# Performance work log

Measured on AMD Instinct MI355X. Metric: run time of the kernel, lower is better.

Reference implementation:

```python
import jax, jax.numpy as jnp
import numpy as np

EMBED_DIM = 1024
NUM_HEADS = 16
HEAD_DIM = EMBED_DIM // NUM_HEADS
MLP_HIDDEN = 4096
B, S = 2, 2048


def setup_inputs() -> dict:
    key = jax.random.key(0)
    ks = jax.random.split(key, 10)
    sd = lambda fan_in: 1.0 / np.sqrt(fan_in)
    x = jax.random.normal(ks[0], (B, S, EMBED_DIM), dtype=jnp.float32)
    # weights stored (in, out) so y = x @ W + b (same math as torch Linear)
    w_qkv = jax.random.normal(ks[1], (EMBED_DIM, 3 * EMBED_DIM), jnp.float32) * sd(EMBED_DIM)
    w_proj = jax.random.normal(ks[2], (EMBED_DIM, EMBED_DIM), jnp.float32) * sd(EMBED_DIM)
    b_proj = jnp.zeros((EMBED_DIM,), jnp.float32)
    w_fc1 = jax.random.normal(ks[3], (EMBED_DIM, MLP_HIDDEN), jnp.float32) * sd(EMBED_DIM)
    b_fc1 = jnp.zeros((MLP_HIDDEN,), jnp.float32)
    w_fc2 = jax.random.normal(ks[4], (MLP_HIDDEN, EMBED_DIM), jnp.float32) * sd(MLP_HIDDEN)
    b_fc2 = jnp.zeros((EMBED_DIM,), jnp.float32)
    g1 = jnp.ones((EMBED_DIM,), jnp.float32)
    be1 = jnp.zeros((EMBED_DIM,), jnp.float32)
    g2 = jnp.ones((EMBED_DIM,), jnp.float32)
    be2 = jnp.zeros((EMBED_DIM,), jnp.float32)
    return {"x": x, "w_qkv": w_qkv, "w_proj": w_proj, "b_proj": b_proj,
            "w_fc1": w_fc1, "b_fc1": b_fc1, "w_fc2": w_fc2, "b_fc2": b_fc2,
            "g1": g1, "be1": be1, "g2": g2, "be2": be2}


def _layernorm(x, g, b, eps=1e-5):
    mu = jnp.mean(x, axis=-1, keepdims=True)
    var = jnp.var(x, axis=-1, keepdims=True)
    return (x - mu) * jax.lax.rsqrt(var + eps) * g + b


def _block(x, w_qkv, w_proj, b_proj, w_fc1, b_fc1, w_fc2, b_fc2, g1, be1, g2, be2):
    # --- attention branch ---
    h = _layernorm(x, g1, be1)
    qkv = h @ w_qkv  # [B,S,3D]
    qkv = qkv.reshape(B, S, 3, NUM_HEADS, HEAD_DIM).transpose(2, 0, 3, 1, 4)
    q, k, v = qkv[0], qkv[1], qkv[2]  # each [B,H,S,Dh]
    scale = 1.0 / np.sqrt(HEAD_DIM).astype(np.float32)
    dots = jnp.einsum('bhqd,bhkd->bhqk', q, k) * scale  # naive full score matrix
    attn = jax.nn.softmax(dots, axis=-1)
    out = jnp.einsum('bhqk,bhkd->bhqd', attn, v)
    out = out.transpose(0, 2, 1, 3).reshape(B, S, EMBED_DIM)
    x = x + (out @ w_proj + b_proj)
    # --- mlp branch ---
    h2 = _layernorm(x, g2, be2)
    mlp = jax.nn.gelu(h2 @ w_fc1 + b_fc1, approximate=False) @ w_fc2 + b_fc2
    return x + mlp


def reference(x, w_qkv, w_proj, b_proj, w_fc1, b_fc1, w_fc2, b_fc2, g1, be1, g2, be2):
    return _block(x, w_qkv, w_proj, b_proj, w_fc1, b_fc1, w_fc2, b_fc2, g1, be1, g2, be2)
```

## Files before the change

kernel.cpp:

```cpp
#include <hip/hip_runtime.h>

typedef __attribute__((ext_vector_type(8))) short short8;
typedef __attribute__((ext_vector_type(4))) float f32x4;

#define MFMA16(a, b, c) __builtin_amdgcn_mfma_f32_16x16x32_bf16((a), (b), (c), 0, 0, 0)

static __device__ __forceinline__ unsigned short f2bf(float f) {
    unsigned int u = __float_as_uint(f);
    return (unsigned short)((u + 0x7fffu + ((u >> 16) & 1u)) >> 16);
}

static __device__ __forceinline__ void glds16(const unsigned short* g, unsigned short* l) {
    __builtin_amdgcn_global_load_lds(
        (const __attribute__((address_space(1))) unsigned int*)g,
        (__attribute__((address_space(3))) unsigned int*)l, 16, 0, 0);
}

__global__ __launch_bounds__(256) void convt_all_kernel(
    const float* __restrict__ w_qkv, const float* __restrict__ w_proj,
    const float* __restrict__ w_fc1, const float* __restrict__ w_fc2,
    unsigned short* __restrict__ wqkvT, unsigned short* __restrict__ wprojT,
    unsigned short* __restrict__ wfc1T, unsigned short* __restrict__ wfc2T) {
    __shared__ unsigned short Ts[32][33];
    int id = blockIdx.x;
    const float* W; unsigned short* WT; int K, N, bx, by;
    if (id < 3072)      { W = w_qkv;  WT = wqkvT;  K = 1024; N = 3072; bx = id % 96;  by = id / 96; }
    else if (id < 4096) { id -= 3072; W = w_proj; WT = wprojT; K = 1024; N = 1024; bx = id & 31; by = id >> 5; }
    else if (id < 8192) { id -= 4096; W = w_fc1;  WT = wfc1T;  K = 1024; N = 4096; bx = id & 127; by = id >> 7; }
    else                { id -= 8192; W = w_fc2;  WT = wfc2T;  K = 4096; N = 1024; bx = id & 31; by = id >> 5; }
    int t = threadIdx.x;
    int bk = by * 32, bn = bx * 32;
    int r = t >> 3, c = (t & 7) * 4;
    float4 w = *(const float4*)&W[(size_t)(bk + r) * N + bn + c];
    Ts[c + 0][r] = f2bf(w.x); Ts[c + 1][r] = f2bf(w.y);
    Ts[c + 2][r] = f2bf(w.z); Ts[c + 3][r] = f2bf(w.w);
    __syncthreads();
    ushort4 o;
    o.x = Ts[r][c]; o.y = Ts[r][c + 1]; o.z = Ts[r][c + 2]; o.w = Ts[r][c + 3];
    *(ushort4*)&WT[(size_t)(bn + r) * K + bk + c] = o;
}

__global__ __launch_bounds__(256) void ln_kernel(const float* __restrict__ x,
                                                 const float* __restrict__ g,
                                                 const float* __restrict__ be,
                                                 unsigned short* __restrict__ y) {
    int row = blockIdx.x;
    const float* xr = x + (size_t)row * 1024;
    unsigned short* yr = y + (size_t)row * 1024;
    int t = threadIdx.x;
    float v[4];
    float sum = 0.f, sq = 0.f;
#pragma unroll
    for (int i = 0; i < 4; ++i) {
        float f = xr[t + i * 256];
        v[i] = f; sum += f; sq += f * f;
    }
#pragma unroll
    for (int o = 32; o > 0; o >>= 1) { sum += __shfl_down(sum, o); sq += __shfl_down(sq, o); }
    __shared__ float red[8];
    int wave = t >> 6, lane = t & 63;
    if (lane == 0) { red[wave] = sum; red[4 + wave] = sq; }
    __syncthreads();
    sum = red[0] + red[1] + red[2] + red[3];
    sq  = red[4] + red[5] + red[6] + red[7];
    float mean = sum * (1.f / 1024.f);
    float var  = sq * (1.f / 1024.f) - mean * mean;
    float rstd = rsqrtf(var + 1e-5f);
#pragma unroll
    for (int i = 0; i < 4; ++i) {
        int c = t + i * 256;
        yr[c] = f2bf((v[i] - mean) * rstd * g[c] + be[c]);
    }
}

__global__ __launch_bounds__(512) void gemm256_kernel(const unsigned short* __restrict__ A,
                                                      const unsigned short* __restrict__ BT,
                                                      const float* __restrict__ bias,
                                                      const float* __restrict__ resid,
                                                      void* __restrict__ C,
                                                      int M, int N, int K, int act, int cF32) {
    __shared__ __align__(16) unsigned short As[4][256][32];
    __shared__ __align__(16) unsigned short Bs[4][256][32];
    int t = threadIdx.x, wave = t >> 6, lane = t & 63;
    int lm = lane & 15, quad = lane >> 4;
    int wm = (wave >> 2) * 128, wn = (wave & 3) * 64;

    int id = blockIdx.y * gridDim.x + blockIdx.x;
    int gsz = gridDim.x * 8;
    int grp = id / gsz, rem = id % gsz;
    int br = (grp * 8 + (rem & 7)) * 256;
    int bc = (rem >> 3) * 256;

    int srow = lane >> 2;
    int scol = ((lane & 3) ^ ((srow >> 1) & 3)) * 8;
    const unsigned short* Ag0 = A + (size_t)(br + wave * 32 + srow) * K + scol;
    const unsigned short* Ag1 = Ag0 + (size_t)16 * K;
    const unsigned short* Bg0 = BT + (size_t)(bc + wave * 32 + srow) * K + scol;
    const unsigned short* Bg1 = Bg0 + (size_t)16 * K;

    f32x4 zero4 = {0.f, 0.f, 0.f, 0.f};
    f32x4 acc[8][4];
#pragma unroll
    for (int i = 0; i < 8; ++i)
#pragma unroll
        for (int j = 0; j < 4; ++j) acc[i][j] = zero4;

    auto stage = [&](int buf, int ko) {
        glds16(Ag0 + ko, &As[buf][wave * 32][0]);
        glds16(Ag1 + ko, &As[buf][wave * 32 + 16][0]);
        glds16(Bg0 + ko, &Bs[buf][wave * 32][0]);
        glds16(Bg1 + ko, &Bs[buf][wave * 32 + 16][0]);
    };

    int nt = K >> 5;
    stage(0, 0);
    stage(1, 32);
    stage(2, 64);
    int cq = (quad ^ ((lm >> 1) & 3)) << 3;
    for (int tt = 0; tt < nt; ++tt) {
        int cur = tt & 3;
        if (tt + 3 < nt) {
            stage((tt + 3) & 3, (tt + 3) << 5);
            asm volatile("s_waitcnt vmcnt(12)" ::: "memory");
        } else if (tt + 2 < nt) {
            asm volatile("s_waitcnt vmcnt(8)" ::: "memory");
        } else if (tt + 1 < nt) {
            asm volatile("s_waitcnt vmcnt(4)" ::: "memory");
        } else {
            asm volatile("s_waitcnt vmcnt(0)" ::: "memory");
        }
        __builtin_amdgcn_s_barrier();
        __builtin_amdgcn_sched_barrier(0);
        short8 af[8], bf[4];
#pragma unroll
        for (int i = 0; i < 8; ++i) af[i] = *(const short8*)&As[cur][wm + i * 16 + lm][cq];
#pragma unroll
        for (int j = 0; j < 4; ++j) bf[j] = *(const short8*)&Bs[cur][wn + j * 16 + lm][cq];
#pragma unroll
        for (int i = 0; i < 8; ++i)
#pragma unroll
            for (int j = 0; j < 4; ++j) acc[i][j] = MFMA16(af[i], bf[j], acc[i][j]);
        __builtin_amdgcn_sched_barrier(0);
        __builtin_amdgcn_s_barrier();
    }

#pragma unroll
    for (int i = 0; i < 8; ++i)
#pragma unroll
        for (int j = 0; j < 4; ++j) {
            int col = bc + wn + j * 16 + lm;
            float bv = bias ? bias[col] : 0.f;
#pragma unroll
            for (int r = 0; r < 4; ++r) {
                int row = br + wm + i * 16 + quad * 4 + r;
                float v = acc[i][j][r] + bv;
                if (act == 1) v = 0.5f * v * (1.f + erff(v * 0.70710678118f));
                size_t idx = (size_t)row * N + col;
                if (resid) v += resid[idx];
                if (cF32) ((float*)C)[idx] = v;
                else ((unsigned short*)C)[idx] = f2bf(v);
            }
        }
}

template <int BN>
__global__ __launch_bounds__(256) void gemm_kernel(const unsigned short* __restrict__ A,
                                                   const unsigned short* __restrict__ BT,
                                                   const float* __restrict__ bias,
                                                   const float* __restrict__ resid,
                                                   void* __restrict__ C,
                                                   int M, int N, int K, int act, int cF32) {
    constexpr int NT = BN / 32;
    __shared__ __align__(16) unsigned short As[2][128][32];
    __shared__ __align__(16) unsigned short Bs[2][BN][32];
    int t = threadIdx.x, wave = t >> 6, lane = t & 63;
    int lm = lane & 15, quad = lane >> 4;
    int wm = (wave >> 1) * 64, wn = (wave & 1) * (BN / 2);

    int id = blockIdx.y * gridDim.x + blockIdx.x;
    int gsz = gridDim.x * 8;
    int grp = id / gsz, rem = id % gsz;
    int br = (grp * 8 + (rem & 7)) * 128;
    int bc = (rem >> 3) * BN;

    int srow = lane >> 2;
    int scol = ((lane & 3) ^ ((srow >> 1) & 3)) * 8;
    const unsigned short* Ag0 = A + (size_t)(br + wave * 32 + srow) * K + scol;
    const unsigned short* Ag1 = Ag0 + (size_t)16 * K;
    const unsigned short* Bg0 = BT + (size_t)(bc + wave * (BN / 4) + srow) * K + scol;
    const unsigned short* Bg1 = Bg0 + (size_t)16 * K;

    f32x4 zero4 = {0.f, 0.f, 0.f, 0.f};
    f32x4 acc[4][NT];
#pragma unroll
    for (int i = 0; i < 4; ++i)
#pragma unroll
        for (int j = 0; j < NT; ++j) acc[i][j] = zero4;

    auto stage = [&](int buf, int ko) {
        glds16(Ag0 + ko, &As[buf][wave * 32][0]);
        glds16(Ag1 + ko, &As[buf][wave * 32 + 16][0]);
        glds16(Bg0 + ko, &Bs[buf][wave * (BN / 4)][0]);
        if (BN == 128) glds16(Bg1 + ko, &Bs[buf][wave * (BN / 4) + 16][0]);
    };

    int nt = K >> 5;
    stage(0, 0);
    int rsw = (lm >> 1) & 3;
    int cq = (quad ^ rsw) << 3;
    for (int tt = 0; tt < nt; ++tt) {
        int cur = tt & 1;
        if (tt + 1 < nt) {
            stage(cur ^ 1, (tt + 1) << 5);
            if (BN == 128) asm volatile("s_waitcnt vmcnt(4)" ::: "memory");
            else           asm volatile("s_waitcnt vmcnt(3)" ::: "memory");
        } else {
            asm volatile("s_waitcnt vmcnt(0)" ::: "memory");
        }
        __builtin_amdgcn_s_barrier();
        __builtin_amdgcn_sched_barrier(0);
        short8 af[4], bf[NT];
#pragma unroll
        for (int i = 0; i < 4; ++i) af[i] = *(const short8*)&As[cur][wm + i * 16 + lm][cq];
#pragma unroll
        for (int j = 0; j < NT; ++j) bf[j] = *(const short8*)&Bs[cur][wn + j * 16 + lm][cq];
#pragma unroll
        for (int i = 0; i < 4; ++i)
#pragma unroll
            for (int j = 0; j < NT; ++j) acc[i][j] = MFMA16(af[i], bf[j], acc[i][j]);
        __builtin_amdgcn_sched_barrier(0);
        __builtin_amdgcn_s_barrier();
    }

#pragma unroll
    for (int i = 0; i < 4; ++i)
#pragma unroll
        for (int j = 0; j < NT; ++j) {
            int col = bc + wn + j * 16 + lm;
            float bv = bias ? bias[col] : 0.f;
#pragma unroll
            for (int r = 0; r < 4; ++r) {
                int row = br + wm + i * 16 + quad * 4 + r;
                float v = acc[i][j][r] + bv;
                if (act == 1) v = 0.5f * v * (1.f + erff(v * 0.70710678118f));
                size_t idx = (size_t)row * N + col;
                if (resid) v += resid[idx];
                if (cF32) ((float*)C)[idx] = v;
                else ((unsigned short*)C)[idx] = f2bf(v);
            }
        }
}

__global__ __launch_bounds__(256) void kvprep_kernel(const unsigned short* __restrict__ qkv,
                                                     unsigned short* __restrict__ Kp,
                                                     unsigned short* __restrict__ Vt) {
    __shared__ unsigned short Vl[64][72];
    int t = threadIdx.x;
    int w = blockIdx.x, bh = blockIdx.y;
    int b = bh >> 4, h = bh & 15;
    int kt = w * 64;
    int sl = t >> 2, c = (t & 3) * 16;
    const unsigned short* src = qkv + (size_t)(b * 2048 + kt + sl) * 3072 + h * 64 + c;
    {
        uint4 k0 = *(const uint4*)(src + 1024);
        uint4 k1 = *(const uint4*)(src + 1024 + 8);
        int sw = sl & 7;
        int o0 = (c >> 3), o1 = o0 + 1;
        unsigned short* krow = Kp + ((size_t)bh * 2048 + kt + sl) * 64;
        *(uint4*)&krow[(o0 ^ sw) << 3] = k0;
        *(uint4*)&krow[(o1 ^ sw) << 3] = k1;
    }
    {
        uint4 v0 = *(const uint4*)(src + 2048);
        uint4 v1 = *(const uint4*)(src + 2048 + 8);
        *(uint4*)&Vl[sl][c] = v0;
        *(uint4*)&Vl[sl][c + 8] = v1;
    }
    __syncthreads();
    {
        int d = t >> 2, kc = (t & 3) * 16;
        unsigned short vv[16];
#pragma unroll
        for (int i = 0; i < 16; ++i) vv[i] = Vl[kc + i][d];
        int sw = d & 7;
        int ko0 = kc >> 3, ko1 = ko0 + 1;
        unsigned short* vrow = Vt + ((((size_t)bh * 32 + w) * 64) + d) * 64;
        *(uint4*)&vrow[(ko0 ^ sw) << 3] = *(uint4*)&vv[0];
        *(uint4*)&vrow[(ko1 ^ sw) << 3] = *(uint4*)&vv[8];
    }
}

__global__ __launch_bounds__(256) void attn2_kernel(const unsigned short* __restrict__ qkv,
                                                    const unsigned short* __restrict__ Kp,
                                                    const unsigned short* __restrict__ Vt,
                                                    unsigned short* __restrict__ out) {
    __shared__ __align__(16) unsigned short Qs[64][72];
    __shared__ __align__(16) unsigned short Ks[4096];
    __shared__ __align__(16) unsigned short Vs[4096];
    __shared__ __align__(16) unsigned short Ps[4][16][72];

    int t = threadIdx.x, wave = t >> 6, lane = t & 63;
    int lm = lane & 15, quad = lane >> 4, k8 = quad * 8;
    int bh = blockIdx.y, b = bh >> 4, h = bh & 15;
    int q0 = blockIdx.x * 64;
    const unsigned short* base = qkv + (size_t)b * 2048 * 3072 + h * 64;

    {
        int r = t >> 2, c = (t & 3) * 16;
        const unsigned short* src = base + (size_t)(q0 + r) * 3072 + c;
        *(uint4*)&Qs[r][c] = *(const uint4*)src;
        *(uint4*)&Qs[r][c + 8] = *(const uint4*)(src + 8);
    }
    __syncthreads();
    short8 qa0 = *(const short8*)&Qs[wave * 16 + lm][k8];
    short8 qa1 = *(const short8*)&Qs[wave * 16 + lm][32 + k8];

    f32x4 zero4 = {0.f, 0.f, 0.f, 0.f};
    f32x4 oacc[4] = {zero4, zero4, zero4, zero4};
    float lsum[4] = {0.f, 0.f, 0.f, 0.f};

    for (int kt = 0; kt < 2048; kt += 64) {
        __syncthreads();
        {
            const unsigned short* kg = Kp + ((size_t)bh * 2048 + kt) * 64 + wave * 1024 + (lane << 3);
            unsigned short* kl = &Ks[wave * 1024];
            glds16(kg, kl);
            glds16(kg + 512, kl + 512);
            const unsigned short* vg = Vt + (((size_t)bh * 32 + (kt >> 6)) * 64) * 64 + wave * 1024 + (lane << 3);
            unsigned short* vl = &Vs[wave * 1024];
            glds16(vg, vl);
            glds16(vg + 512, vl + 512);
        }
        __syncthreads();

        f32x4 s[4];
#pragma unroll
        for (int nt = 0; nt < 4; ++nt) {
            int key = nt * 16 + lm;
            int swk = lm & 7;
            const unsigned short* krow = &Ks[key * 64];
            short8 kf0 = *(const short8*)&krow[(quad ^ swk) << 3];
            short8 kf1 = *(const short8*)&krow[((quad ^ swk) ^ 4) << 3];
            f32x4 a = zero4;
            a = MFMA16(qa0, kf0, a);
            a = MFMA16(qa1, kf1, a);
            s[nt] = a;
        }

#pragma unroll
        for (int r = 0; r < 4; ++r) {
            int row = quad * 4 + r;
            int sw = (row >> 1) & 7;
#pragma unroll
            for (int nt = 0; nt < 4; ++nt) {
                float p = __expf(s[nt][r] * 0.125f - 8.0f);
                lsum[r] += p;
                int g = (nt << 1) + (lm >> 3);
                Ps[wave][row][((g ^ sw) << 3) + (lm & 7)] = f2bf(p);
            }
        }

#pragma unroll
        for (int kh = 0; kh < 2; ++kh) {
            int pg = (kh << 2) + quad;
            short8 pa = *(const short8*)&Ps[wave][lm][(pg ^ ((lm >> 1) & 7)) << 3];
#pragma unroll
            for (int nt = 0; nt < 4; ++nt) {
                int d = nt * 16 + lm;
                short8 vf = *(const short8*)&Vs[d * 64 + ((pg ^ (lm & 7)) << 3)];
                oacc[nt] = MFMA16(pa, vf, oacc[nt]);
            }
        }
    }

#pragma unroll
    for (int r = 0; r < 4; ++r) {
        float l = lsum[r];
        l += __shfl_xor(l, 1); l += __shfl_xor(l, 2);
        l += __shfl_xor(l, 4); l += __shfl_xor(l, 8);
        float inv = 1.f / l;
        int qrow = q0 + wave * 16 + quad * 4 + r;
        size_t o = ((size_t)(b * 2048 + qrow)) * 1024 + h * 64;
#pragma unroll
        for (int nt = 0; nt < 4; ++nt) out[o + nt * 16 + lm] = f2bf(oacc[nt][r] * inv);
    }
}

__global__ __launch_bounds__(256) void attn_kernel(const unsigned short* __restrict__ qkv,
                                                   unsigned short* __restrict__ out) {
    __shared__ __align__(16) unsigned short Qs[64][72];
    __shared__ __align__(16) unsigned short Ks[64][72];
    __shared__ __align__(16) unsigned short Vs[64][72];
    __shared__ __align__(16) unsigned short Ps[4][16][72];
    int t = threadIdx.x, wave = t >> 6, lane = t & 63;
    int lm = lane & 15, quad = lane >> 4, k8 = quad * 8;
    int bh = blockIdx.y, b = bh >> 4, h = bh & 15;
    int q0 = blockIdx.x * 64;
    const unsigned short* base = qkv + (size_t)b * 2048 * 3072 + h * 64;
    const unsigned short* kb = base + 1024;
    const unsigned short* vb = base + 2048;
    {
        int r = t >> 2, c = (t & 3) * 16;
        const unsigned short* src = base + (size_t)(q0 + r) * 3072 + c;
        *(uint4*)&Qs[r][c] = *(const uint4*)src;
        *(uint4*)&Qs[r][c + 8] = *(const uint4*)(src + 8);
    }
    __syncthreads();
    short8 qa0 = *(const short8*)&Qs[wave * 16 + lm][k8];
    short8 qa1 = *(const short8*)&Qs[wave * 16 + lm][32 + k8];
    f32x4 zero4 = {0.f, 0.f, 0.f, 0.f};
    f32x4 oacc[4] = {zero4, zero4, zero4, zero4};
    float lsum[4] = {0.f, 0.f, 0.f, 0.f};
    int sr = t >> 2, sc = (t & 3) * 16;
    for (int kt = 0; kt < 2048; kt += 64) {
        __syncthreads();
        {
            const unsigned short* ksrc = kb + (size_t)(kt + sr) * 3072 + sc;
            *(uint4*)&Ks[sr][sc] = *(const uint4*)ksrc;
            *(uint4*)&Ks[sr][sc + 8] = *(const uint4*)(ksrc + 8);
            const unsigned short* vsrc = vb + (size_t)(kt + sr) * 3072 + sc;
            unsigned short tv[16] __attribute__((aligned(16)));
            *(uint4*)&tv[0] = *(const uint4*)vsrc;
            *(uint4*)&tv[8] = *(const uint4*)(vsrc + 8);
            int kg = sr >> 3, kw = sr & 7;
#pragma unroll
            for (int j = 0; j < 16; ++j) {
                int d = sc + j;
                Vs[d][((kg ^ ((d >> 3) & 7)) << 3) + kw] = tv[j];
            }
        }
        __syncthreads();
        f32x4 s[4];
#pragma unroll
        for (int nt = 0; nt < 4; ++nt) {
            short8 kf0 = *(const short8*)&Ks[nt * 16 + lm][k8];
            short8 kf1 = *(const short8*)&Ks[nt * 16 + lm][32 + k8];
            f32x4 a = zero4;
            a = MFMA16(qa0, kf0, a);
            a = MFMA16(qa1, kf1, a);
            s[nt] = a;
        }
#pragma unroll
        for (int r = 0; r < 4; ++r) {
            int row = quad * 4 + r;
            int sw = (row >> 1) & 7;
#pragma unroll
            for (int nt = 0; nt < 4; ++nt) {
                float p = __expf(s[nt][r] * 0.125f - 8.0f);
                lsum[r] += p;
                int g = (nt << 1) + (lm >> 3);
                Ps[wave][row][((g ^ sw) << 3) + (lm & 7)] = f2bf(p);
            }
        }
#pragma unroll
        for (int kh = 0; kh < 2; ++kh) {
            int pg = (kh << 2) + quad;
            short8 pa = *(const short8*)&Ps[wave][lm][(pg ^ ((lm >> 1) & 7)) << 3];
#pragma unroll
            for (int nt = 0; nt < 4; ++nt) {
                int d = nt * 16 + lm;
                short8 vf = *(const short8*)&Vs[d][(pg ^ ((d >> 3) & 7)) << 3];
                oacc[nt] = MFMA16(pa, vf, oacc[nt]);
            }
        }
    }
#pragma unroll
    for (int r = 0; r < 4; ++r) {
        float l = lsum[r];
        l += __shfl_xor(l, 1); l += __shfl_xor(l, 2);
        l += __shfl_xor(l, 4); l += __shfl_xor(l, 8);
        float inv = 1.f / l;
        int qrow = q0 + wave * 16 + quad * 4 + r;
        size_t o = ((size_t)(b * 2048 + qrow)) * 1024 + h * 64;
#pragma unroll
        for (int nt = 0; nt < 4; ++nt) out[o + nt * 16 + lm] = f2bf(oacc[nt][r] * inv);
    }
}

extern "C" void kernel_launch(void* const* d_in, const int* in_sizes, int n_in,
                              void* d_out, int out_size, void* d_ws, size_t ws_size,
                              hipStream_t stream) {
    const float* x      = (const float*)d_in[0];
    const float* w_qkv  = (const float*)d_in[1];
    const float* w_proj = (const float*)d_in[2];
    const float* b_proj = (const float*)d_in[3];
    const float* w_fc1  = (const float*)d_in[4];
    const float* b_fc1  = (const float*)d_in[5];
    const float* w_fc2  = (const float*)d_in[6];
    const float* b_fc2  = (const float*)d_in[7];
    const float* g1     = (const float*)d_in[8];
    const float* be1    = (const float*)d_in[9];
    const float* g2     = (const float*)d_in[10];
    const float* be2    = (const float*)d_in[11];
    float* out = (float*)d_out;
    unsigned short* sb = (unsigned short*)d_out;

    char* ws = (char*)d_ws;
    unsigned short* wqkvT  = (unsigned short*)ws;
    unsigned short* wprojT = (unsigned short*)(ws + ((size_t)6u << 20));
    unsigned short* wfc1T  = (unsigned short*)(ws + ((size_t)8u << 20));
    unsigned short* wfc2T  = (unsigned short*)(ws + ((size_t)16u << 20));
    unsigned short* qkv    = (unsigned short*)(ws + ((size_t)24u << 20));

    convt_all_kernel<<<dim3(12288), dim3(256), 0, stream>>>(
        w_qkv, w_proj, w_fc1, w_fc2, wqkvT, wprojT, wfc1T, wfc2T);
    ln_kernel<<<dim3(4096), dim3(256), 0, stream>>>(x, g1, be1, sb);
    gemm256_kernel<<<dim3(12, 16), dim3(512), 0, stream>>>(
        sb, wqkvT, nullptr, nullptr, qkv, 4096, 3072, 1024, 0, 0);

    if (ws_size >= ((size_t)72u << 20)) {
        unsigned short* Kp = (unsigned short*)(ws + ((size_t)48u << 20));
        unsigned short* Vt = (unsigned short*)(ws + ((size_t)56u << 20));
        float*          x2 = (float*)(ws + ((size_t)24u << 20));
        unsigned short* m1 = (unsigned short*)(ws + ((size_t)40u << 20));
        kvprep_kernel<<<dim3(32, 32), dim3(256), 0, stream>>>(qkv, Kp, Vt);
        attn2_kernel<<<dim3(32, 32), dim3(256), 0, stream>>>(qkv, Kp, Vt, sb);
        gemm_kernel<64><<<dim3(16, 32), dim3(256), 0, stream>>>(
            sb, wprojT, b_proj, x, x2, 4096, 1024, 1024, 0, 1);
        ln_kernel<<<dim3(4096), dim3(256), 0, stream>>>(x2, g2, be2, sb);
        gemm256_kernel<<<dim3(16, 16), dim3(512), 0, stream>>>(
            sb, wfc1T, b_fc1, nullptr, m1, 4096, 4096, 1024, 1, 0);
        gemm_kernel<64><<<dim3(16, 32), dim3(256), 0, stream>>>(
            m1, wfc2T, b_fc2, x2, out, 4096, 1024, 4096, 0, 1);
    } else {
        float*          x2  = (float*)(ws + ((size_t)24u << 20));
        unsigned short* m1c = (unsigned short*)(ws + ((size_t)40u << 20));
        unsigned short* h2  = (unsigned short*)d_out + ((size_t)4u << 20);
        attn_kernel<<<dim3(32, 32), dim3(256), 0, stream>>>(qkv, sb);
        gemm_kernel<64><<<dim3(16, 32), dim3(256), 0, stream>>>(
            sb, wprojT, b_proj, x, x2, 4096, 1024, 1024, 0, 1);
        ln_kernel<<<dim3(4096), dim3(256), 0, stream>>>(x2, g2, be2, h2);
        for (int c = 0; c < 4; ++c) {
            size_t ro = (size_t)c * 1024;
            gemm_kernel<128><<<dim3(32, 8), dim3(256), 0, stream>>>(
                h2 + ro * 1024, wfc1T, b_fc1, nullptr, m1c, 1024, 4096, 1024, 1, 0);
            gemm_kernel<64><<<dim3(16, 8), dim3(256), 0, stream>>>(
                m1c, wfc2T, b_fc2, x2 + ro * 1024, out + ro * 1024, 1024, 1024, 4096, 0, 1);
        }
    }
}
```

Before: 451.4 us.

## Restructure GEMM main loop into four-phase ping-pong with 64-wide K tiles

The 256x256 GEMM mainloop moves from a 4-deep 32-wide K-tile ring buffer to a 2-buffer 64-wide K tile. Each tile is split into four quadrant MFMA phases, with LDS fragment reads and global-to-LDS loads for the next tile interleaved between them. s_setprio raises wave priority during the MFMA bursts, and launch bounds request 2 blocks per CU. The aim is to overlap memory traffic with matrix math and cut barrier stalls per K step. The cost is more barriers per tile and tighter register pressure, which could spill under the occupancy hint.

```diff
diff --git a/kernel.cpp b/kernel.cpp
--- a/kernel.cpp
+++ b/kernel.cpp
@@ -73,14 +73,25 @@
     }
 }
 
-__global__ __launch_bounds__(512) void gemm256_kernel(const unsigned short* __restrict__ A,
-                                                      const unsigned short* __restrict__ BT,
-                                                      const float* __restrict__ bias,
-                                                      const float* __restrict__ resid,
-                                                      void* __restrict__ C,
-                                                      int M, int N, int K, int act, int cF32) {
-    __shared__ __align__(16) unsigned short As[4][256][32];
-    __shared__ __align__(16) unsigned short Bs[4][256][32];
+#define PHASE_MID                                            \
+    __builtin_amdgcn_sched_barrier(0);                       \
+    __builtin_amdgcn_s_barrier();                            \
+    asm volatile("s_waitcnt lgkmcnt(0)" ::: "memory");       \
+    __builtin_amdgcn_sched_barrier(0);                       \
+    __builtin_amdgcn_s_setprio(1);
+#define PHASE_END                                            \
+    __builtin_amdgcn_s_setprio(0);                           \
+    __builtin_amdgcn_sched_barrier(0);                       \
+    __builtin_amdgcn_s_barrier();
+
+__global__ __launch_bounds__(512, 2) void gemm256_kernel(const unsigned short* __restrict__ A,
+                                                         const unsigned short* __restrict__ BT,
+                                                         const float* __restrict__ bias,
+                                                         const float* __restrict__ resid,
+                                                         void* __restrict__ C,
+                                                         int M, int N, int K, int act, int cF32) {
+    __shared__ __align__(16) unsigned short As[2][2][256][32];
+    __shared__ __align__(16) unsigned short Bs[2][2][256][32];
     int t = threadIdx.x, wave = t >> 6, lane = t & 63;
     int lm = lane & 15, quad = lane >> 4;
     int wm = (wave >> 2) * 128, wn = (wave & 3) * 64;
@@ -93,10 +104,19 @@
 
     int srow = lane >> 2;
     int scol = ((lane & 3) ^ ((srow >> 1) & 3)) * 8;
-    const unsigned short* Ag0 = A + (size_t)(br + wave * 32 + srow) * K + scol;
-    const unsigned short* Ag1 = Ag0 + (size_t)16 * K;
-    const unsigned short* Bg0 = BT + (size_t)(bc + wave * 32 + srow) * K + scol;
-    const unsigned short* Bg1 = Bg0 + (size_t)16 * K;
+    const unsigned short* Ag = A + (size_t)(br + wave * 16 + srow) * K + scol;
+    const unsigned short* Bg = BT + (size_t)(bc + wave * 16 + srow) * K + scol;
+
+    auto stA = [&](int p_, int half, int ko) {
+        const unsigned short* g = Ag + (size_t)half * 128 * K + ko;
+        glds16(g,      &As[p_][0][half * 128 + wave * 16][0]);
+        glds16(g + 32, &As[p_][1][half * 128 + wave * 16][0]);
+    };
+    auto stB = [&](int p_, int half, int ko) {
+        const unsigned short* g = Bg + (size_t)half * 128 * K + ko;
+        glds16(g,      &Bs[p_][0][half * 128 + wave * 16][0]);
+        glds16(g + 32, &Bs[p_][1][half * 128 + wave * 16][0]);
+    };
 
     f32x4 zero4 = {0.f, 0.f, 0.f, 0.f};
     f32x4 acc[8][4];
@@ -105,43 +125,88 @@
 #pragma unroll
         for (int j = 0; j < 4; ++j) acc[i][j] = zero4;
 
-    auto stage = [&](int buf, int ko) {
-        glds16(Ag0 + ko, &As[buf][wave * 32][0]);
-        glds16(Ag1 + ko, &As[buf][wave * 32 + 16][0]);
-        glds16(Bg0 + ko, &Bs[buf][wave * 32][0]);
-        glds16(Bg1 + ko, &Bs[buf][wave * 32 + 16][0]);
-    };
-
-    int nt = K >> 5;
-    stage(0, 0);
-    stage(1, 32);
-    stage(2, 64);
+    int ntile = K >> 6;
+    stA(0, 0, 0); stA(0, 1, 0); stB(0, 0, 0); stB(0, 1, 0);
+    if (ntile > 1) { stB(1, 0, 64); stA(1, 0, 64); }
+    __builtin_amdgcn_sched_barrier(0);
+    if (ntile > 1) asm volatile("s_waitcnt vmcnt(4)" ::: "memory");
+    else           asm volatile("s_waitcnt vmcnt(0)" ::: "memory");
+    __builtin_amdgcn_s_barrier();
+
     int cq = (quad ^ ((lm >> 1) & 3)) << 3;
-    for (int tt = 0; tt < nt; ++tt) {
-        int cur = tt & 3;
-        if (tt + 3 < nt) {
-            stage((tt + 3) & 3, (tt + 3) << 5);
-            asm volatile("s_waitcnt vmcnt(12)" ::: "memory");
-        } else if (tt + 2 < nt) {
-            asm volatile("s_waitcnt vmcnt(8)" ::: "memory");
-        } else if (tt + 1 < nt) {
-            asm volatile("s_waitcnt vmcnt(4)" ::: "memory");
-        } else {
-            asm volatile("s_waitcnt vmcnt(0)" ::: "memory");
-        }
+
+    for (int tt = 0; tt < ntile; ++tt) {
+        int p = tt & 1, q = p ^ 1;
+        int tko = tt * 64;
+        short8 aLo0[4], aLo1[4], bLo0[2], bLo1[2];
+#pragma unroll
+        for (int i = 0; i < 4; ++i) {
+            aLo0[i] = *(const short8*)&As[p][0][wm + i * 16 + lm][cq];
+            aLo1[i] = *(const short8*)&As[p][1][wm + i * 16 + lm][cq];
+        }
+#pragma unroll
+        for (int j = 0; j < 2; ++j) {
+            bLo0[j] = *(const short8*)&Bs[p][0][wn + j * 16 + lm][cq];
+            bLo1[j] = *(const short8*)&Bs[p][1][wn + j * 16 + lm][cq];
+        }
+        if (tt + 1 < ntile) stB(q, 1, tko + 64);
+        PHASE_MID;
+#pragma unroll
+        for (int i = 0; i < 4; ++i)
+#pragma unroll
+            for (int j = 0; j < 2; ++j) {
+                acc[i][j] = MFMA16(aLo0[i], bLo0[j], acc[i][j]);
+                acc[i][j] = MFMA16(aLo1[i], bLo1[j], acc[i][j]);
+            }
+        PHASE_END;
+        short8 bHi0[2], bHi1[2];
+#pragma unroll
+        for (int j = 0; j < 2; ++j) {
+            bHi0[j] = *(const short8*)&Bs[p][0][wn + 32 + j * 16 + lm][cq];
+            bHi1[j] = *(const short8*)&Bs[p][1][wn + 32 + j * 16 + lm][cq];
+        }
+        if (tt + 1 < ntile) stA(q, 1, tko + 64);
+        PHASE_MID;
+#pragma unroll
+        for (int i = 0; i < 4; ++i)
+#pragma unroll
+            for (int j = 0; j < 2; ++j) {
+                acc[i][j + 2] = MFMA16(aLo0[i], bHi0[j], acc[i][j + 2]);
+                acc[i][j + 2] = MFMA16(aLo1[i], bHi1[j], acc[i][j + 2]);
+            }
+        PHASE_END;
+        short8 aHi0[4], aHi1[4];
+#pragma unroll
+        for (int i = 0; i < 4; ++i) {
+            aHi0[i] = *(const short8*)&As[p][0][wm + 64 + i * 16 + lm][cq];
+            aHi1[i] = *(const short8*)&As[p][1][wm + 64 + i * 16 + lm][cq];
+        }
+        if (tt + 2 < ntile) stB(p, 0, tko + 128);
+        PHASE_MID;
+#pragma unroll
+        for (int i = 0; i < 4; ++i)
+#pragma unroll
+            for (int j = 0; j < 2; ++j) {
+                acc[i + 4][j] = MFMA16(aHi0[i], bLo0[j], acc[i + 4][j]);
+                acc[i + 4][j] = MFMA16(aHi1[i], bLo1[j], acc[i + 4][j]);
+            }
+        PHASE_END;
+        if (tt + 2 < ntile) stA(p, 0, tko + 128);
+        __builtin_amdgcn_sched_barrier(0);
+        if (tt + 2 < ntile) asm volatile("s_waitcnt vmcnt(4)" ::: "memory");
+        else                asm volatile("s_waitcnt vmcnt(0)" ::: "memory");
         __builtin_amdgcn_s_barrier();
+        asm volatile("s_waitcnt lgkmcnt(0)" ::: "memory");
         __builtin_amdgcn_sched_barrier(0);
-        short8 af[8], bf[4];
-#pragma unroll
-        for (int i = 0; i < 8; ++i) af[i] = *(const short8*)&As[cur][wm + i * 16 + lm][cq];
-#pragma unroll
-        for (int j = 0; j < 4; ++j) bf[j] = *(const short8*)&Bs[cur][wn + j * 16 + lm][cq];
-#pragma unroll
-        for (int i = 0; i < 8; ++i)
-#pragma unroll
-            for (int j = 0; j < 4; ++j) acc[i][j] = MFMA16(af[i], bf[j], acc[i][j]);
-        __builtin_amdgcn_sched_barrier(0);
-        __builtin_amdgcn_s_barrier();
+        __builtin_amdgcn_s_setprio(1);
+#pragma unroll
+        for (int i = 0; i < 4; ++i)
+#pragma unroll
+            for (int j = 0; j < 2; ++j) {
+                acc[i + 4][j + 2] = MFMA16(aHi0[i], bHi0[j], acc[i + 4][j + 2]);
+                acc[i + 4][j + 2] = MFMA16(aHi1[i], bHi1[j], acc[i + 4][j + 2]);
+            }
+        PHASE_END;
     }
 
 #pragma unroll
```

After: 426.6 us. 5.5% less time.
